# Optimization experiments

Measured on AMD Instinct MI355X. Metric: run time of the kernel, lower is better.

Reference implementation:

```python
import jax, jax.numpy as jnp
import numpy as np

B = 8192
I_SIZE = 1024
H_SIZE = 1024
C2 = 2.7183  # module's hard-coded e approximation

def setup_inputs() -> dict:
    key = jax.random.key(0)
    k0, k1, k2, k3, k4 = jax.random.split(key, 5)
    input_tensor = jax.random.uniform(k0, (B, I_SIZE + 1), dtype=jnp.float32)  # last col = dt >= 0
    h_cur = jax.random.normal(k1, (B, H_SIZE), dtype=jnp.float32)
    c_cur = jax.random.normal(k2, (B, H_SIZE), dtype=jnp.float32)
    W_layers = jax.random.normal(k3, (4 * H_SIZE, I_SIZE + H_SIZE), dtype=jnp.float32) * 0.02
    b_layers = jnp.zeros((4 * H_SIZE,), dtype=jnp.float32)
    W_desc = jax.random.normal(k4, (H_SIZE, H_SIZE), dtype=jnp.float32) * 0.02
    b_desc = jnp.zeros((H_SIZE,), dtype=jnp.float32)
    return {"input_tensor": input_tensor, "h_cur": h_cur, "c_cur": c_cur,
            "W_layers": W_layers, "b_layers": b_layers,
            "W_desc": W_desc, "b_desc": b_desc}

def reference(input_tensor, h_cur, c_cur, W_layers, b_layers, W_desc, b_desc):
    x = input_tensor[:, :-1]          # [B, I]
    dt = input_tensor[:, -1:]         # [B, 1]
    # map_elapse_time: T = 1/log(t + e), broadcast over h_size (matmul with ones == broadcast)
    T = 1.0 / jnp.log(dt + C2)        # [B, 1]
    C_ST = jnp.tanh(h_cur @ W_desc.T + b_desc)          # [B, H]
    h_adj = h_cur - C_ST + T * C_ST                     # decayed short-term memory
    combined = jnp.concatenate([x, h_adj], axis=1)      # [B, I+H]
    gates = combined @ W_layers.T + b_layers            # [B, 4H]
    cc_i, cc_f, cc_o, cc_g = jnp.split(gates, 4, axis=1)
    i = jax.nn.sigmoid(cc_i)
    f = jax.nn.sigmoid(cc_f)
    o = jax.nn.sigmoid(cc_o)
    g = jnp.tanh(cc_g)
    c_next = f * c_cur + i * g
    h_next = o * jnp.tanh(c_next)
    return (h_next, c_next)
```

## Files before the change

### kernel.cpp

```cpp
#include <hip/hip_runtime.h>
#include <hip/hip_bf16.h>
#include <math.h>

typedef __bf16 bf16x8 __attribute__((ext_vector_type(8)));
typedef float  f32x4  __attribute__((ext_vector_type(4)));

#define B_ROWS 8192
#define HSZ    1024

#define GLOAD16(gsrc, ldst)                                                          \
  __builtin_amdgcn_global_load_lds((const __attribute__((address_space(1))) void*)(gsrc), \
                                   (__attribute__((address_space(3))) void*)(ldst),  \
                                   16, 0, 0)

__device__ inline unsigned short f2bf(float f) {
  union { float f; unsigned u; } x; x.f = f;
  unsigned r = x.u + 0x7fffu + ((x.u >> 16) & 1u);
  return (unsigned short)(r >> 16);
}

__device__ inline void store4bf(unsigned short* p, float4 v) {
  ushort4 u;
  u.x = f2bf(v.x); u.y = f2bf(v.y); u.z = f2bf(v.z); u.w = f2bf(v.w);
  *(ushort4*)p = u;
}

__device__ inline float sigm(float x) { return 1.0f / (1.0f + __expf(-x)); }

__global__ void k_convert(const float* __restrict__ inp,
                          const float* __restrict__ h,
                          const float* __restrict__ Wl,
                          const float* __restrict__ Wd,
                          unsigned short* __restrict__ comb,
                          unsigned short* __restrict__ Wlb,
                          unsigned short* __restrict__ hb,
                          unsigned short* __restrict__ Wdb,
                          float* __restrict__ Tm1) {
  const long stride = (long)gridDim.x * blockDim.x;
  const long tid0 = (long)blockIdx.x * blockDim.x + threadIdx.x;

  for (long i = tid0; i < (long)B_ROWS * HSZ / 4; i += stride) {
    float4 v = ((const float4*)h)[i];
    store4bf(hb + i * 4, v);
  }
  for (long i = tid0; i < (long)B_ROWS * HSZ / 4; i += stride) {
    long e = i * 4; long b = e >> 10; long c = e & 1023;
    float4 v = *(const float4*)(inp + b * 1025 + c);
    store4bf(comb + b * 2048 + c, v);
  }
  for (long i = tid0; i < 4096L * 2048 / 4; i += stride) {
    float4 v = ((const float4*)Wl)[i];
    store4bf(Wlb + i * 4, v);
  }
  for (long i = tid0; i < 1024L * 1024 / 4; i += stride) {
    float4 v = ((const float4*)Wd)[i];
    store4bf(Wdb + i * 4, v);
  }
  for (long i = tid0; i < B_ROWS; i += stride) {
    float dt = inp[i * 1025 + 1024];
    Tm1[i] = 1.0f / logf(dt + 2.7183f) - 1.0f;
  }
}

__global__ void k_gemm1(const unsigned short* __restrict__ A,
                        const unsigned short* __restrict__ Bm,
                        const float* __restrict__ h,
                        const float* __restrict__ bd,
                        const float* __restrict__ Tm1,
                        unsigned short* __restrict__ comb) {
  const int K = 1024;
  __shared__ __align__(16) unsigned short As[128 * 32];
  __shared__ __align__(16) unsigned short Bs[128 * 32];
  const int tid = threadIdx.x;
  const int lane = tid & 63;
  const int wave = tid >> 6;
  const int wr = wave >> 1, wc = wave & 1;
  const int bRow = blockIdx.x;
  const int bCol = blockIdx.y;

  const int sRow = tid >> 2;
  const int sK = (tid & 3) * 8;
  const unsigned short* aSrc0 = A + (long)(bRow * 128 + sRow) * K + sK;
  const unsigned short* aSrc1 = A + (long)(bRow * 128 + 64 + sRow) * K + sK;
  const unsigned short* bSrc0 = Bm + (long)(bCol * 128 + sRow) * K + sK;
  const unsigned short* bSrc1 = Bm + (long)(bCol * 128 + 64 + sRow) * K + sK;
  unsigned short* aDst0 = As + tid * 8;
  unsigned short* aDst1 = As + 2048 + tid * 8;
  unsigned short* bDst0 = Bs + tid * 8;
  unsigned short* bDst1 = Bs + 2048 + tid * 8;

  f32x4 acc[4][4] = {};
  const int fr = lane & 15, fk = (lane >> 4) * 8;

  for (int k0 = 0; k0 < K; k0 += 32) {
    GLOAD16(aSrc0 + k0, aDst0);
    GLOAD16(aSrc1 + k0, aDst1);
    GLOAD16(bSrc0 + k0, bDst0);
    GLOAD16(bSrc1 + k0, bDst1);
    __syncthreads();
    bf16x8 a[4], b[4];
#pragma unroll
    for (int m = 0; m < 4; m++) a[m] = *(const bf16x8*)(As + (wr * 64 + m * 16 + fr) * 32 + fk);
#pragma unroll
    for (int n = 0; n < 4; n++) b[n] = *(const bf16x8*)(Bs + (wc * 64 + n * 16 + fr) * 32 + fk);
#pragma unroll
    for (int m = 0; m < 4; m++)
#pragma unroll
      for (int n = 0; n < 4; n++)
        acc[m][n] = __builtin_amdgcn_mfma_f32_16x16x32_bf16(a[m], b[n], acc[m][n], 0, 0, 0);
    __syncthreads();
  }

  const int cr = (lane >> 4) * 4;
  const int cc = lane & 15;
#pragma unroll
  for (int m = 0; m < 4; m++)
#pragma unroll
    for (int n = 0; n < 4; n++) {
      const int col = bCol * 128 + wc * 64 + n * 16 + cc;
#pragma unroll
      for (int r = 0; r < 4; r++) {
        const int row = bRow * 128 + wr * 64 + m * 16 + cr + r;
        float v = acc[m][n][r] + bd[col];
        float cst = tanhf(v);
        float hadj = h[(long)row * HSZ + col] + Tm1[row] * cst;
        comb[(long)row * 2048 + 1024 + col] = f2bf(hadj);
      }
    }
}

#define NT2 64
__global__ __launch_bounds__(512, 2)
void k_gemm2_pipe(const unsigned short* __restrict__ A,
                  const unsigned short* __restrict__ Bm,
                  const float* __restrict__ bl,
                  const float* __restrict__ c_cur,
                  float* __restrict__ out) {
  __shared__ __align__(16) unsigned short lds[4][16384];

  const int tid = threadIdx.x;
  const int lane = tid & 63;
  const int wid = tid >> 6;
  const int wr = wid >> 2;
  const int wc = wid & 3;

  const int bid = blockIdx.x;
  const int xcd = bid & 7;
  const int ii = bid >> 3;
  const int sweep = ii >> 5;
  const int pos = ii & 31;
  const int bRow = xcd * 4 + sweep * 2 + (pos & 1);
  const int bCol = pos >> 1;

  const int sr = tid >> 2;
  const int swsel = (sr >> 1) & 3;
  const int gk = ((tid & 3) ^ swsel) << 3;
  const unsigned short* aBase = A + (long)(bRow * 256 + sr) * 2048 + gk;
  const int rl0 = sr, rl1 = 128 + sr;
  const int grow0 = ((rl0 >> 4) & 3) * 1024 + bCol * 64 + (rl0 >> 6) * 16 + (rl0 & 15);
  const int grow1 = ((rl1 >> 4) & 3) * 1024 + bCol * 64 + (rl1 >> 6) * 16 + (rl1 & 15);
  const unsigned short* bBase0 = Bm + (long)grow0 * 2048 + gk;
  const unsigned short* bBase1 = Bm + (long)grow1 * 2048 + gk;

#define STAGE_A2(tt) { unsigned short* d_ = &lds[(tt) & 3][0] + tid * 8;          \
    GLOAD16(aBase + (long)(tt) * 32, d_);                                          \
    GLOAD16(aBase + 128L * 2048 + (long)(tt) * 32, d_ + 512 * 8); }
#define STAGE_B2(tt) { unsigned short* d_ = &lds[(tt) & 3][8192] + tid * 8;       \
    GLOAD16(bBase0 + (long)(tt) * 32, d_);                                         \
    GLOAD16(bBase1 + (long)(tt) * 32, d_ + 512 * 8); }

  const int fr = lane & 15, q = lane >> 4;
  int offA[8], offB[4];
#pragma unroll
  for (int m = 0; m < 8; m++) {
    const int row = wr * 128 + m * 16 + fr;
    offA[m] = row * 32 + ((q ^ ((row >> 1) & 3)) << 3);
  }
#pragma unroll
  for (int n = 0; n < 4; n++) {
    const int row = wc * 64 + n * 16 + fr;
    offB[n] = 8192 + row * 32 + ((q ^ ((row >> 1) & 3)) << 3);
  }

  f32x4 acc[8][4] = {};
  bf16x8 aL0[4], aL1[4], b0[4], b1[4], aH[4];

  STAGE_A2(0); STAGE_B2(0);
  STAGE_A2(1); STAGE_B2(1);
  STAGE_A2(2); STAGE_B2(2);
  asm volatile("s_waitcnt vmcnt(8)" ::: "memory");
  __builtin_amdgcn_sched_barrier(0);
  __builtin_amdgcn_s_barrier();
  __builtin_amdgcn_sched_barrier(0);
#pragma unroll
  for (int m = 0; m < 4; m++) aL0[m] = *(const bf16x8*)(&lds[0][0] + offA[m]);
#pragma unroll
  for (int n = 0; n < 4; n++) b0[n] = *(const bf16x8*)(&lds[0][0] + offB[n]);

#define TILE_BODY(t, aC, bC, aN, bN)                                                 \
  {                                                                                  \
    const unsigned short* buf = lds[(t) & 3];                                        \
    _Pragma("unroll")                                                                \
    for (int m = 0; m < 4; m++) aH[m] = *(const bf16x8*)(buf + offA[m + 4]);         \
    if ((t) < NT2 - 3) STAGE_A2((t) + 3);                                            \
    __builtin_amdgcn_sched_barrier(0);                                               \
    __builtin_amdgcn_s_setprio(1);                                                   \
    _Pragma("unroll")                                                                \
    for (int m = 0; m < 4; m++)                                                      \
      _Pragma("unroll")                                                              \
      for (int n = 0; n < 4; n++)                                                    \
        acc[m][n] = __builtin_amdgcn_mfma_f32_16x16x32_bf16(aC[m], bC[n], acc[m][n], 0, 0, 0); \
    __builtin_amdgcn_s_setprio(0);                                                   \
    asm volatile("s_waitcnt lgkmcnt(0)" ::: "memory");                               \
    if ((t) < NT2 - 3)        { asm volatile("s_waitcnt vmcnt(6)" ::: "memory"); }   \
    else if ((t) == NT2 - 3)  { asm volatile("s_waitcnt vmcnt(4)" ::: "memory"); }   \
    else                      { asm volatile("s_waitcnt vmcnt(0)" ::: "memory"); }   \
    __builtin_amdgcn_sched_barrier(0);                                               \
    __builtin_amdgcn_s_barrier();                                                    \
    __builtin_amdgcn_sched_barrier(0);                                               \
    if ((t) < NT2 - 1) {                                                             \
      const unsigned short* bufN = lds[((t) + 1) & 3];                               \
      _Pragma("unroll")                                                              \
      for (int m = 0; m < 4; m++) aN[m] = *(const bf16x8*)(bufN + offA[m]);          \
      _Pragma("unroll")                                                              \
      for (int n = 0; n < 4; n++) bN[n] = *(const bf16x8*)(bufN + offB[n]);          \
      if ((t) < NT2 - 3) STAGE_B2((t) + 3);                                          \
    }                                                                                \
    __builtin_amdgcn_sched_barrier(0);                                               \
    __builtin_amdgcn_s_setprio(1);                                                   \
    _Pragma("unroll")                                                                \
    for (int m = 0; m < 4; m++)                                                      \
      _Pragma("unroll")                                                              \
      for (int n = 0; n < 4; n++)                                                    \
        acc[m + 4][n] = __builtin_amdgcn_mfma_f32_16x16x32_bf16(aH[m], bC[n], acc[m + 4][n], 0, 0, 0); \
    __builtin_amdgcn_s_setprio(0);                                                   \
  }

  for (int t = 0; t < NT2; t += 2) {
    TILE_BODY(t,     aL0, b0, aL1, b1);
    TILE_BODY(t + 1, aL1, b1, aL0, b0);
  }
#undef TILE_BODY

  const int cr = (lane >> 4) * 4;
  const int cc = lane & 15;
  const int j = bCol * 64 + wc * 16 + cc;
#pragma unroll
  for (int m = 0; m < 8; m++) {
#pragma unroll
    for (int r = 0; r < 4; r++) {
      const int row = bRow * 256 + wr * 128 + m * 16 + cr + r;
      float iv = sigm(acc[m][0][r] + bl[j]);
      float fv = sigm(acc[m][1][r] + bl[1024 + j]);
      float ov = sigm(acc[m][2][r] + bl[2048 + j]);
      float gv = tanhf(acc[m][3][r] + bl[3072 + j]);
      float cn = fv * c_cur[(long)row * HSZ + j] + iv * gv;
      float hn = ov * tanhf(cn);
      out[(long)row * HSZ + j] = hn;
      out[(long)B_ROWS * HSZ + (long)row * HSZ + j] = cn;
    }
  }
}

extern "C" void kernel_launch(void* const* d_in, const int* in_sizes, int n_in,
                              void* d_out, int out_size, void* d_ws, size_t ws_size,
                              hipStream_t stream) {
  const float* inp = (const float*)d_in[0];
  const float* h   = (const float*)d_in[1];
  const float* c   = (const float*)d_in[2];
  const float* Wl  = (const float*)d_in[3];
  const float* bl  = (const float*)d_in[4];
  const float* Wd  = (const float*)d_in[5];
  const float* bd  = (const float*)d_in[6];

  char* ws = (char*)d_ws;
  unsigned short* comb = (unsigned short*)(ws);
  unsigned short* Wlb  = (unsigned short*)(ws + 33554432);
  unsigned short* hb   = (unsigned short*)(ws + 50331648);
  unsigned short* Wdb  = (unsigned short*)(ws + 67108864);
  float*          Tm1  = (float*)(ws + 69206016);
  float*          out  = (float*)d_out;

  hipLaunchKernelGGL(k_convert, dim3(2048), dim3(256), 0, stream,
                     inp, h, Wl, Wd, comb, Wlb, hb, Wdb, Tm1);
  hipLaunchKernelGGL(k_gemm1, dim3(64, 8), dim3(256), 0, stream,
                     hb, Wdb, h, bd, Tm1, comb);
  hipLaunchKernelGGL(k_gemm2_pipe, dim3(512), dim3(512), 0, stream,
                     comb, Wlb, bl, c, out);
}
```

Measured before the change: 227.4 us.

## Restructure gemm2 main loop to one barrier per tile with full-fragment loads

Replaces the hand-interleaved half-tile MFMA schedule, which used register double-buffered fragments and explicit lgkmcnt waits, with a simpler loop. Each tile now does one vmcnt wait and one barrier, issues the next stage's global-to-LDS loads, reads all 8 A and 4 B fragments, and then runs 32 MFMAs. The intent is to cut barrier and scheduling overhead and let the compiler overlap the LDS reads with MFMAs. The cost is that LDS-read latency is no longer software-pipelined across tiles, and register pressure per tile goes up.

```diff
diff --git a/kernel.cpp b/kernel.cpp
--- a/kernel.cpp
+++ b/kernel.cpp
@@ -131,11 +131,11 @@
 
 #define NT2 64
 __global__ __launch_bounds__(512, 2)
-void k_gemm2_pipe(const unsigned short* __restrict__ A,
-                  const unsigned short* __restrict__ Bm,
-                  const float* __restrict__ bl,
-                  const float* __restrict__ c_cur,
-                  float* __restrict__ out) {
+void k_gemm2_fr(const unsigned short* __restrict__ A,
+                const unsigned short* __restrict__ Bm,
+                const float* __restrict__ bl,
+                const float* __restrict__ c_cur,
+                float* __restrict__ out) {
   __shared__ __align__(16) unsigned short lds[4][16384];
 
   const int tid = threadIdx.x;
@@ -162,10 +162,10 @@
   const unsigned short* bBase0 = Bm + (long)grow0 * 2048 + gk;
   const unsigned short* bBase1 = Bm + (long)grow1 * 2048 + gk;
 
-#define STAGE_A2(tt) { unsigned short* d_ = &lds[(tt) & 3][0] + tid * 8;          \
+#define STAGE_A2(slot, tt) { unsigned short* d_ = &lds[slot][0] + tid * 8;        \
     GLOAD16(aBase + (long)(tt) * 32, d_);                                          \
     GLOAD16(aBase + 128L * 2048 + (long)(tt) * 32, d_ + 512 * 8); }
-#define STAGE_B2(tt) { unsigned short* d_ = &lds[(tt) & 3][8192] + tid * 8;       \
+#define STAGE_B2(slot, tt) { unsigned short* d_ = &lds[slot][8192] + tid * 8;     \
     GLOAD16(bBase0 + (long)(tt) * 32, d_);                                         \
     GLOAD16(bBase1 + (long)(tt) * 32, d_ + 512 * 8); }
 
@@ -183,64 +183,42 @@
   }
 
   f32x4 acc[8][4] = {};
-  bf16x8 aL0[4], aL1[4], b0[4], b1[4], aH[4];
-
-  STAGE_A2(0); STAGE_B2(0);
-  STAGE_A2(1); STAGE_B2(1);
-  STAGE_A2(2); STAGE_B2(2);
-  asm volatile("s_waitcnt vmcnt(8)" ::: "memory");
-  __builtin_amdgcn_sched_barrier(0);
-  __builtin_amdgcn_s_barrier();
-  __builtin_amdgcn_sched_barrier(0);
-#pragma unroll
-  for (int m = 0; m < 4; m++) aL0[m] = *(const bf16x8*)(&lds[0][0] + offA[m]);
-#pragma unroll
-  for (int n = 0; n < 4; n++) b0[n] = *(const bf16x8*)(&lds[0][0] + offB[n]);
-
-#define TILE_BODY(t, aC, bC, aN, bN)                                                 \
+
+  STAGE_A2(0, 0); STAGE_B2(0, 0);
+  STAGE_A2(1, 1); STAGE_B2(1, 1);
+  STAGE_A2(2, 2); STAGE_B2(2, 2);
+
+#define BODY(t, SLOT, VM, DOSTAGE)                                                   \
   {                                                                                  \
-    const unsigned short* buf = lds[(t) & 3];                                        \
+    asm volatile("s_waitcnt vmcnt(" #VM ")" ::: "memory");                           \
+    __builtin_amdgcn_s_barrier();                                                    \
+    if (DOSTAGE) { STAGE_A2(((t) + 3) & 3, (t) + 3); STAGE_B2(((t) + 3) & 3, (t) + 3); } \
+    const unsigned short* buf = &lds[SLOT][0];                                       \
+    bf16x8 aF[8], bF[4];                                                             \
     _Pragma("unroll")                                                                \
-    for (int m = 0; m < 4; m++) aH[m] = *(const bf16x8*)(buf + offA[m + 4]);         \
-    if ((t) < NT2 - 3) STAGE_A2((t) + 3);                                            \
-    __builtin_amdgcn_sched_barrier(0);                                               \
+    for (int n = 0; n < 4; n++) bF[n] = *(const bf16x8*)(buf + offB[n]);             \
+    _Pragma("unroll")                                                                \
+    for (int m = 0; m < 8; m++) aF[m] = *(const bf16x8*)(buf + offA[m]);             \
     __builtin_amdgcn_s_setprio(1);                                                   \
     _Pragma("unroll")                                                                \
-    for (int m = 0; m < 4; m++)                                                      \
+    for (int m = 0; m < 8; m++)                                                      \
       _Pragma("unroll")                                                              \
       for (int n = 0; n < 4; n++)                                                    \
-        acc[m][n] = __builtin_amdgcn_mfma_f32_16x16x32_bf16(aC[m], bC[n], acc[m][n], 0, 0, 0); \
+        acc[m][n] = __builtin_amdgcn_mfma_f32_16x16x32_bf16(aF[m], bF[n], acc[m][n], 0, 0, 0); \
     __builtin_amdgcn_s_setprio(0);                                                   \
-    asm volatile("s_waitcnt lgkmcnt(0)" ::: "memory");                               \
-    if ((t) < NT2 - 3)        { asm volatile("s_waitcnt vmcnt(6)" ::: "memory"); }   \
-    else if ((t) == NT2 - 3)  { asm volatile("s_waitcnt vmcnt(4)" ::: "memory"); }   \
-    else                      { asm volatile("s_waitcnt vmcnt(0)" ::: "memory"); }   \
-    __builtin_amdgcn_sched_barrier(0);                                               \
-    __builtin_amdgcn_s_barrier();                                                    \
-    __builtin_amdgcn_sched_barrier(0);                                               \
-    if ((t) < NT2 - 1) {                                                             \
-      const unsigned short* bufN = lds[((t) + 1) & 3];                               \
-      _Pragma("unroll")                                                              \
-      for (int m = 0; m < 4; m++) aN[m] = *(const bf16x8*)(bufN + offA[m]);          \
-      _Pragma("unroll")                                                              \
-      for (int n = 0; n < 4; n++) bN[n] = *(const bf16x8*)(bufN + offB[n]);          \
-      if ((t) < NT2 - 3) STAGE_B2((t) + 3);                                          \
-    }                                                                                \
-    __builtin_amdgcn_sched_barrier(0);                                               \
-    __builtin_amdgcn_s_setprio(1);                                                   \
-    _Pragma("unroll")                                                                \
-    for (int m = 0; m < 4; m++)                                                      \
-      _Pragma("unroll")                                                              \
-      for (int n = 0; n < 4; n++)                                                    \
-        acc[m + 4][n] = __builtin_amdgcn_mfma_f32_16x16x32_bf16(aH[m], bC[n], acc[m + 4][n], 0, 0, 0); \
-    __builtin_amdgcn_s_setprio(0);                                                   \
-  }
-
-  for (int t = 0; t < NT2; t += 2) {
-    TILE_BODY(t,     aL0, b0, aL1, b1);
-    TILE_BODY(t + 1, aL1, b1, aL0, b0);
-  }
-#undef TILE_BODY
+  }
+
+  for (int t = 0; t < 60; t += 4) {
+    BODY(t,     0, 8, true);
+    BODY(t + 1, 1, 8, true);
+    BODY(t + 2, 2, 8, true);
+    BODY(t + 3, 3, 8, true);
+  }
+  BODY(60, 0, 8, true);
+  BODY(61, 1, 8, false);
+  BODY(62, 2, 4, false);
+  BODY(63, 3, 0, false);
+#undef BODY
 
   const int cr = (lane >> 4) * 4;
   const int cc = lane & 15;
@@ -285,6 +263,6 @@
                      inp, h, Wl, Wd, comb, Wlb, hb, Wdb, Tm1);
   hipLaunchKernelGGL(k_gemm1, dim3(64, 8), dim3(256), 0, stream,
                      hb, Wdb, h, bd, Tm1, comb);
-  hipLaunchKernelGGL(k_gemm2_pipe, dim3(512), dim3(512), 0, stream,
+  hipLaunchKernelGGL(k_gemm2_fr, dim3(512), dim3(512), 0, stream,
                      comb, Wlb, bl, c, out);
 }
```

New measurement: 226.2 us. No clear change (-0.5%).
